# Performance work log

Hardware: AMD Instinct MI355X
Metric: run time of the kernel (lower is better)

## Reference

```python
import jax, jax.numpy as jnp
import numpy as np

K = 9
VOCAB = 7
DIM = 512
LOW = 256  # downsampled bottleneck dim
N_LAYERS = 2
EPS = 1e-5


def _inorm(x, g, b):
    # InstanceNorm1d over length axis (biased var), x: (N, C, K)
    m = jnp.mean(x, axis=-1, keepdims=True)
    v = jnp.mean((x - m) ** 2, axis=-1, keepdims=True)
    return g[None, :, None] * (x - m) * jax.lax.rsqrt(v + EPS) + b[None, :, None]


def _conv5_same(x, w, b):
    # x: (N, C, K), w: (O, C, 5), dilation 1, padding 'same' -> pad 2
    y = jax.lax.conv_general_dilated(
        x, w, window_strides=(1,), padding=[(2, 2)],
        dimension_numbers=('NCH', 'OIH', 'NCH'))
    return y + b[None, :, None]


def _bytenet_layer(x, p):
    (g1, b1, g2, b2, g3, b3, w1, c1b, w2, c2b, w3, c3b) = p
    h = jax.nn.gelu(_inorm(x, g1, b1), approximate=False)
    h = jnp.einsum('nck,oc->nok', h, w1) + c1b[None, :, None]      # 1x1 conv 512->256
    h = jax.nn.gelu(_inorm(h, g2, b2), approximate=False)
    h = _conv5_same(h, w2, c2b)                                     # k=5 conv 256->256
    h = jax.nn.gelu(_inorm(h, g3, b3), approximate=False)
    h = jnp.einsum('nck,oc->nok', h, w3) + c3b[None, :, None]      # 1x1 conv 256->512
    return h + x  # dropout is identity in eval


def setup_inputs() -> dict:
    key = jax.random.key(0)
    ks = jax.random.split(key, 16)
    x = jax.random.randint(ks[0], (8, 2048), 0, VOCAB)
    emb = jax.random.normal(ks[1], (VOCAB, DIM), jnp.float32) * 0.02
    emb = emb.at[6].set(0.0)  # padding_idx=6
    d = {
        'x': x,
        'emb': emb,
        'ln1_w': jnp.ones((N_LAYERS, DIM)), 'ln1_b': jnp.zeros((N_LAYERS, DIM)),
        'ln2_w': jnp.ones((N_LAYERS, LOW)), 'ln2_b': jnp.zeros((N_LAYERS, LOW)),
        'ln3_w': jnp.ones((N_LAYERS, LOW)), 'ln3_b': jnp.zeros((N_LAYERS, LOW)),
        'c1_w': jax.random.normal(ks[2], (N_LAYERS, LOW, DIM), jnp.float32) * 0.02,
        'c1_b': jnp.zeros((N_LAYERS, LOW)),
        'c2_w': jax.random.normal(ks[3], (N_LAYERS, LOW, LOW, 5), jnp.float32) * 0.02,
        'c2_b': jnp.zeros((N_LAYERS, LOW)),
        'c3_w': jax.random.normal(ks[4], (N_LAYERS, DIM, LOW), jnp.float32) * 0.02,
        'c3_b': jnp.zeros((N_LAYERS, DIM)),
        'out_w': jax.random.normal(ks[5], (VOCAB, DIM * K), jnp.float32) * 0.02,
        'out_b': jnp.zeros((VOCAB,)),
    }
    return d


def reference(x, emb, ln1_w, ln1_b, ln2_w, ln2_b, ln3_w, ln3_b,
              c1_w, c1_b, c2_w, c2_b, c3_w, c3_b, out_w, out_b):
    B, L = x.shape
    W = L - K + 1
    e = emb[x]                                        # (B, L, D)
    idx = jnp.arange(W)[:, None] + jnp.arange(K)      # (W, K)
    win = e[:, idx, :]                                # (B, W, K, D)
    h = win.transpose(0, 1, 3, 2).reshape(B * W, DIM, K)  # (N, D, K)
    for i in range(N_LAYERS):
        p = (ln1_w[i], ln1_b[i], ln2_w[i], ln2_b[i], ln3_w[i], ln3_b[i],
             c1_w[i], c1_b[i], c2_w[i], c2_b[i], c3_w[i], c3_b[i])
        h = _bytenet_layer(h, p)
    pred = h.reshape(B * W, DIM * K) @ out_w.T + out_b
    return pred.reshape(B, W, VOCAB)
```

## Files before the change

### kernel.cpp

```cpp
#include <hip/hip_runtime.h>

typedef __attribute__((ext_vector_type(8))) short bfv8;
typedef __attribute__((ext_vector_type(4))) float f32x4;
typedef __attribute__((ext_vector_type(4))) unsigned short usv4;

typedef __attribute__((address_space(1))) const void gvoid;
typedef __attribute__((address_space(3))) void lvoid;
__device__ __forceinline__ void gload16(const void* g, void* l) {
  __builtin_amdgcn_global_load_lds((gvoid*)g, (lvoid*)l, 16, 0, 0);
}

__device__ __forceinline__ float bf2f(unsigned short u) {
  union { unsigned int i; float f; } c; c.i = ((unsigned int)u) << 16; return c.f;
}
__device__ __forceinline__ unsigned short f2bf(float f) {
  union { float f; unsigned int i; } c; c.f = f;
  unsigned int r = c.i + 0x7FFFu + ((c.i >> 16) & 1u);
  return (unsigned short)(r >> 16);
}
__device__ __forceinline__ float gelu_(float x) {
  float z2 = 1.5957691216057308f * x * __builtin_fmaf(0.044715f, x * x, 1.0f);
  float e = __expf(z2);
  float t = __builtin_amdgcn_rcpf(e + 1.0f);
  return x - x * t;
}
__device__ __forceinline__ int div9(int col) {
  return (int)(__umulhi((unsigned)col, 954437177u) >> 1);
}

#define CHP 132
#define CHP2 66

__global__ void k_prep(const float* c1w, const float* c2w, const float* c3w,
                       const float* outw, unsigned short* W1b, unsigned short* W2t,
                       unsigned short* W3b, float* OWt) {
  int i = blockIdx.x * 256 + threadIdx.x;
  if (i < 262144) { W1b[i] = f2bf(c1w[i]); return; }
  i -= 262144;
  if (i < 655360) {
    int ii = i & 255, o = (i >> 8) & 255, rest = i >> 16;
    int t = rest % 5, l = rest / 5;
    W2t[i] = f2bf(c2w[(((l * 256 + o) << 8) + ii) * 5 + t]);
    return;
  }
  i -= 655360;
  if (i < 262144) { W3b[i] = f2bf(c3w[i]); return; }
  i -= 262144;
  if (i < 32256) {
    int c = i & 511, rk = i >> 9;
    int r = rk / 9, k = rk - 9 * r;
    OWt[i] = outw[r * 4608 + c * 9 + k];
  }
}

__global__ void k_pinit(const float* outb, float* pred) {
  int i = blockIdx.x * 256 + threadIdx.x;
  if (i < 114240) pred[i] = outb[i % 7];
}

__global__ void k_x0(const int* x, const float* emb, unsigned short* X, int n0) {
  int idx = blockIdx.x * 256 + threadIdx.x;
  int c4 = idx & 127, nl = idx >> 7;
  int gn = n0 + nl, b = gn >> 11, w = gn & 2047;
  unsigned short* dst = X + (size_t)(12 + nl * 12) * 512 + (c4 << 2);
  const int* xb = x + (b << 11);
  #pragma unroll
  for (int k = 0; k < 9; k++) {
    int t = w + k; if (t > 2047) t = 2047;
    const float* e = emb + xb[t] * 512 + (c4 << 2);
    float4 ev = *(const float4*)e;
    usv4 pk;
    pk[0] = f2bf(ev.x); pk[1] = f2bf(ev.y);
    pk[2] = f2bf(ev.z); pk[3] = f2bf(ev.w);
    *(usv4*)(dst + k * 512) = pk;
  }
}

__global__ void k_zpad(unsigned short* AL) {
  int i = threadIdx.x;
  for (; i < 12 * 256; i += 256) AL[i] = 0;
}

template <int MODE>
__global__ __launch_bounds__(512, 2) void k_gemm(
    const unsigned short* __restrict__ Aw, const unsigned short* __restrict__ Bsrc,
    const float* __restrict__ n1w, const float* __restrict__ n1b,
    const float* __restrict__ gw, const float* __restrict__ gb,
    unsigned short* __restrict__ Out, int nkc) {
  __shared__ __align__(16) unsigned short smem[69632];
  unsigned short* sE = smem;

  const int KROW = (MODE == 0) ? 512 : 256;
  const int KSTEPS = (MODE == 1) ? 20 : 8;
  int tid = threadIdx.x, wv = tid >> 6, ln = tid & 63;
  int lr = ln >> 3, lu = ln & 7;
  int swz = (lu ^ lr) << 3;
  int w0 = blockIdx.x << 5;
  int col0 = blockIdx.x * 288;

  int brow[5];
  #pragma unroll
  for (int s = 0; s < 5; s++) {
    int colg = col0 + (s << 6) + (wv << 3) + lr;
    if (colg >= nkc) colg = nkc - 1;
    brow[s] = colg + 3 * div9(colg) + 12;
  }

  f32x4 acc[4][9];
  #pragma unroll
  for (int i = 0; i < 4; i++)
    #pragma unroll
    for (int j = 0; j < 9; j++) acc[i][j] = (f32x4){0.f, 0.f, 0.f, 0.f};

  auto stage = [&](int buf, int ks) {
    int kb, dlt; const unsigned short* Ab;
    if (MODE == 1) {
      int t = ks % 5; kb = (ks / 5) << 6; dlt = t - 2; Ab = Aw + t * 65536;
    } else { kb = ks << 6; dlt = 0; Ab = Aw; }
    unsigned short* cA = smem + buf * 16384;
    unsigned short* cB = smem + 32768 + buf * 18432;
    #pragma unroll
    for (int p = 0; p < 4; p++) {
      int m = (p << 6) + (wv << 3) + lr;
      gload16(Ab + (size_t)m * KROW + kb + swz, cA + (p << 12) + (wv << 9));
    }
    #pragma unroll
    for (int s = 0; s < 4; s++)
      gload16(Bsrc + (size_t)(brow[s] + dlt) * KROW + kb + swz,
              cB + (s << 12) + (wv << 9));
    if (wv < 4)
      gload16(Bsrc + (size_t)(brow[4] + dlt) * KROW + kb + swz,
              cB + (4 << 12) + (wv << 9));
  };

  stage(0, 0);
  __syncthreads();

  int cur = 0;
  for (int ks = 0; ks < KSTEPS; ks++) {
    unsigned short* cA = smem + cur * 16384;
    unsigned short* cB = smem + 32768 + cur * 18432;

    if (MODE == 0) {
      int cg = tid & 15, win = tid >> 4;
      int u = cg >> 1, sub = (cg & 1) << 3;
      int gch = (ks << 6) + (cg << 2);
      float v[9][4], s1[4] = {0.f, 0.f, 0.f, 0.f};
      #pragma unroll
      for (int k = 0; k < 9; k++) {
        int cl = win * 9 + k;
        usv4 rv = *(const usv4*)((char*)cB + cl * 128 + ((u ^ (cl & 7)) << 4) + sub);
        #pragma unroll
        for (int j = 0; j < 4; j++) { v[k][j] = bf2f(rv[j]); s1[j] += v[k][j]; }
      }
      float mn[4], rr[4], gg[4], bo[4];
      #pragma unroll
      for (int j = 0; j < 4; j++) {
        mn[j] = s1[j] * (1.0f / 9.0f);
        float q = 0.f;
        #pragma unroll
        for (int k = 0; k < 9; k++) { float d = v[k][j] - mn[j]; q += d * d; }
        rr[j] = rsqrtf(q * (1.0f / 9.0f) + 1e-5f);
        gg[j] = n1w[gch + j]; bo[j] = n1b[gch + j];
      }
      #pragma unroll
      for (int k = 0; k < 9; k++) {
        int cl = win * 9 + k;
        usv4 pk;
        #pragma unroll
        for (int j = 0; j < 4; j++)
          pk[j] = f2bf(gelu_(gg[j] * (v[k][j] - mn[j]) * rr[j] + bo[j]));
        *(usv4*)((char*)cB + cl * 128 + ((u ^ (cl & 7)) << 4) + sub) = pk;
      }
      __syncthreads();
    }

    if (ks + 1 < KSTEPS) stage(cur ^ 1, ks + 1);

    int l16 = ln & 15, loct = ln >> 4;
    int wm = wv >> 1, wn = wv & 1;
    #pragma unroll
    for (int kk = 0; kk < 2; kk++) {
      int kbyte = (kk << 6) + (loct << 4);
      bfv8 af[4], bf_[9];
      #pragma unroll
      for (int mi = 0; mi < 4; mi++) {
        int row = (wm << 6) + (mi << 4) + l16;
        af[mi] = *(const bfv8*)((const char*)cA + row * 128 + (kbyte ^ ((row & 7) << 4)));
      }
      #pragma unroll
      for (int ni = 0; ni < 9; ni++) {
        int row = wn * 144 + (ni << 4) + l16;
        bf_[ni] = *(const bfv8*)((const char*)cB + row * 128 + (kbyte ^ ((row & 7) << 4)));
      }
      #pragma unroll
      for (int mi = 0; mi < 4; mi++)
        #pragma unroll
        for (int ni = 0; ni < 9; ni++)
          acc[mi][ni] = __builtin_amdgcn_mfma_f32_16x16x32_bf16(
              af[mi], bf_[ni], acc[mi][ni], 0, 0, 0);
    }
    __syncthreads();
    cur ^= 1;
  }

  int l16 = ln & 15, loct = ln >> 4;
  #pragma unroll
  for (int R = 0; R < 2; R++) {
    if (R) __syncthreads();
    if ((wv >> 2) == R) {
      int chh = (((wv >> 1) & 1) << 6) + (loct << 2);
      int colb = (wv & 1) * 144 + l16;
      #pragma unroll
      for (int mi = 0; mi < 4; mi++) {
        #pragma unroll
        for (int ni = 0; ni < 9; ni++) {
          usv4 pk;
          #pragma unroll
          for (int q = 0; q < 4; q++) pk[q] = f2bf(acc[mi][ni][q]);
          *(usv4*)(sE + (colb + (ni << 4)) * CHP + chh + (mi << 4)) = pk;
        }
      }
    }
    __syncthreads();
    #pragma unroll
    for (int tt = 0; tt < 2; tt++) {
      int t = tid + tt * 512;
      int c4 = t & 31, win = t >> 5;
      int chl = (R << 7) + (c4 << 2);
      const unsigned short* sb = sE + (win * 9) * CHP + (c4 << 2);
      size_t ob = (size_t)(12 + (size_t)(w0 + win) * 12) * 256 + chl;
      float s1[4] = {0.f, 0.f, 0.f, 0.f}, s2[4] = {0.f, 0.f, 0.f, 0.f};
      #pragma unroll
      for (int k = 0; k < 9; k++) {
        usv4 rv = *(const usv4*)(sb + k * CHP);
        #pragma unroll
        for (int j = 0; j < 4; j++) {
          float f = bf2f(rv[j]);
          s1[j] += f; s2[j] = __builtin_fmaf(f, f, s2[j]);
        }
      }
      float mn[4], rr[4], gg[4], bo[4];
      #pragma unroll
      for (int j = 0; j < 4; j++) {
        mn[j] = s1[j] * (1.0f / 9.0f);
        float var = s2[j] * (1.0f / 9.0f) - mn[j] * mn[j];
        rr[j] = rsqrtf(var + 1e-5f);
        gg[j] = gw[chl + j]; bo[j] = gb[chl + j];
      }
      #pragma unroll
      for (int k = 0; k < 9; k++) {
        usv4 rv = *(const usv4*)(sb + k * CHP);
        usv4 pk;
        #pragma unroll
        for (int j = 0; j < 4; j++)
          pk[j] = f2bf(gelu_(gg[j] * (bf2f(rv[j]) - mn[j]) * rr[j] + bo[j]));
        *(usv4*)(Out + ob + k * 256) = pk;
      }
      if (MODE == 0) {
        usv4 z = (usv4){0, 0, 0, 0};
        *(usv4*)(Out + ob + 9 * 256) = z;
        *(usv4*)(Out + ob + 10 * 256) = z;
        *(usv4*)(Out + ob + 11 * 256) = z;
      }
    }
  }
}

template <bool FOUT>
__global__ __launch_bounds__(256, 2) void k_gemm2(
    const unsigned short* __restrict__ Aw, const unsigned short* __restrict__ Bsrc,
    const float* __restrict__ cbias, unsigned short* __restrict__ Out, int nkc,
    const float* __restrict__ OWt, float* __restrict__ pred, int n0) {
  __shared__ __align__(16) unsigned short smem[34816];
  unsigned short* sE = smem;
  float* owl = (float*)((char*)smem + 19008);

  const int KROW = 256, KSTEPS = 4;
  int tid = threadIdx.x, wv = tid >> 6, ln = tid & 63;
  int lr = ln >> 3, lu = ln & 7;
  int swz = (lu ^ lr) << 3;
  int id = blockIdx.x;
  int slab = (id >> 3) & 3;
  int tile = ((id >> 5) << 3) | (id & 7);
  int m0 = slab << 7;
  int w0 = tile << 4;
  int col0 = tile * 144;

  int brow[5];
  #pragma unroll
  for (int s = 0; s < 5; s++) {
    int cl = (s < 4) ? ((s << 5) + (wv << 3) + lr) : (128 + (wv << 3) + lr);
    int colg = col0 + cl;
    if (colg >= nkc) colg = nkc - 1;
    brow[s] = colg + 3 * div9(colg) + 12;
  }
  const unsigned short* A0 = Aw + (size_t)m0 * KROW;

  f32x4 acc[2][9];
  #pragma unroll
  for (int i = 0; i < 2; i++)
    #pragma unroll
    for (int j = 0; j < 9; j++) acc[i][j] = (f32x4){0.f, 0.f, 0.f, 0.f};

  auto stage = [&](int buf, int ks) {
    int kb = ks << 6;
    unsigned short* cA = smem + buf * 8192;
    unsigned short* cB = smem + 16384 + buf * 9216;
    #pragma unroll
    for (int p = 0; p < 4; p++) {
      int m = (p << 5) + (wv << 3) + lr;
      gload16(A0 + (size_t)m * KROW + kb + swz, cA + ((p << 5) + (wv << 3)) * 64);
    }
    #pragma unroll
    for (int s = 0; s < 4; s++)
      gload16(Bsrc + (size_t)brow[s] * KROW + kb + swz,
              cB + ((s << 5) + (wv << 3)) * 64);
    if (wv < 2)
      gload16(Bsrc + (size_t)brow[4] * KROW + kb + swz,
              cB + (128 + (wv << 3)) * 64);
  };

  stage(0, 0);
  __syncthreads();

  int cur = 0;
  for (int ks = 0; ks < KSTEPS; ks++) {
    unsigned short* cA = smem + cur * 8192;
    unsigned short* cB = smem + 16384 + cur * 9216;
    if (ks + 1 < KSTEPS) stage(cur ^ 1, ks + 1);

    int l16 = ln & 15, loct = ln >> 4;
    #pragma unroll
    for (int kk = 0; kk < 2; kk++) {
      int kbyte = (kk << 6) + (loct << 4);
      bfv8 af[2], bf_[9];
      #pragma unroll
      for (int mi = 0; mi < 2; mi++) {
        int row = (wv << 5) + (mi << 4) + l16;
        af[mi] = *(const bfv8*)((const char*)cA + row * 128 + (kbyte ^ ((row & 7) << 4)));
      }
      #pragma unroll
      for (int ni = 0; ni < 9; ni++) {
        int row = (ni << 4) + l16;
        bf_[ni] = *(const bfv8*)((const char*)cB + row * 128 + (kbyte ^ ((row & 7) << 4)));
      }
      #pragma unroll
      for (int mi = 0; mi < 2; mi++)
        #pragma unroll
        for (int ni = 0; ni < 9; ni++)
          acc[mi][ni] = __builtin_amdgcn_mfma_f32_16x16x32_bf16(
              af[mi], bf_[ni], acc[mi][ni], 0, 0, 0);
    }
    __syncthreads();
    cur ^= 1;
  }

  if (FOUT) {
    #pragma unroll
    for (int i = 0; i < 8; i++) {
      int c = (i << 8) + tid;
      if (c < 2016)
        gload16(OWt + (size_t)(c >> 5) * 512 + m0 + ((c & 31) << 2),
                (char*)owl + c * 16);
    }
  }

  int l16 = ln & 15, loct = ln >> 4;
  int c4 = tid & 15, win = tid >> 4;
  #pragma unroll
  for (int R = 0; R < 2; R++) {
    if (R) __syncthreads();
    if ((wv >> 1) == R) {
      int chh = ((wv & 1) << 5) + (loct << 2);
      #pragma unroll
      for (int mi = 0; mi < 2; mi++) {
        #pragma unroll
        for (int ni = 0; ni < 9; ni++) {
          usv4 pk;
          #pragma unroll
          for (int q = 0; q < 4; q++) pk[q] = f2bf(acc[mi][ni][q]);
          *(usv4*)(sE + ((ni << 4) + l16) * CHP2 + chh + (mi << 4)) = pk;
        }
      }
    }
    __syncthreads();
    {
      int chg = m0 + (R << 6) + (c4 << 2);
      const unsigned short* sb = sE + (win * 9) * CHP2 + (c4 << 2);
      size_t ob = (size_t)(12 + (size_t)(w0 + win) * 12) * 512 + chg;
      float cb[4];
      #pragma unroll
      for (int j = 0; j < 4; j++) cb[j] = cbias[chg + j];
      if (!FOUT) {
        #pragma unroll
        for (int k = 0; k < 9; k++) {
          usv4 rv = *(const usv4*)(sb + k * CHP2);
          usv4 old = *(usv4*)(Out + ob + k * 512);
          usv4 pk;
          #pragma unroll
          for (int j = 0; j < 4; j++)
            pk[j] = f2bf(bf2f(rv[j]) + cb[j] + bf2f(old[j]));
          *(usv4*)(Out + ob + k * 512) = pk;
        }
      } else {
        float v[9][4];
        #pragma unroll
        for (int k = 0; k < 9; k++) {
          usv4 rv = *(const usv4*)(sb + k * CHP2);
          usv4 old = *(usv4*)(Out + ob + k * 512);
          #pragma unroll
          for (int j = 0; j < 4; j++)
            v[k][j] = bf2f(rv[j]) + cb[j] + bf2f(old[j]);
        }
        int gn = n0 + w0 + win, b = gn >> 11, w = gn & 2047;
        int cho = (R << 6) + (c4 << 2);
        #pragma unroll
        for (int r = 0; r < 7; r++) {
          float p = 0.f;
          #pragma unroll
          for (int k = 0; k < 9; k++) {
            float4 wvv = *(const float4*)(owl + (r * 9 + k) * 128 + cho);
            p = __builtin_fmaf(v[k][0], wvv.x, p);
            p = __builtin_fmaf(v[k][1], wvv.y, p);
            p = __builtin_fmaf(v[k][2], wvv.z, p);
            p = __builtin_fmaf(v[k][3], wvv.w, p);
          }
          p += __shfl_xor(p, 1);
          p += __shfl_xor(p, 2);
          p += __shfl_xor(p, 4);
          p += __shfl_xor(p, 8);
          if (c4 == 0 && w < 2040)
            atomicAdd(pred + (size_t)(b * 2040 + w) * 7 + r, p);
        }
      }
    }
  }
}

extern "C" void kernel_launch(void* const* d_in, const int* in_sizes, int n_in,
                              void* d_out, int out_size, void* d_ws, size_t ws_size,
                              hipStream_t stream) {
  const int*   x    = (const int*)d_in[0];
  const float* emb  = (const float*)d_in[1];
  const float* ln1w = (const float*)d_in[2];
  const float* ln1b = (const float*)d_in[3];
  const float* ln2w = (const float*)d_in[4];
  const float* ln2b = (const float*)d_in[5];
  const float* ln3w = (const float*)d_in[6];
  const float* ln3b = (const float*)d_in[7];
  const float* c1w  = (const float*)d_in[8];
  const float* c2w  = (const float*)d_in[10];
  const float* c3w  = (const float*)d_in[12];
  const float* c3b  = (const float*)d_in[13];
  const float* outw = (const float*)d_in[14];
  const float* outb = (const float*)d_in[15];
  float* pred = (float*)d_out;

  int nc = 8192;
  while (nc > 128 &&
         2488320ull + (unsigned long long)(nc + 1) * 24576ull > ws_size)
    nc >>= 1;
  int nkc = nc * 9;
  int tiles288 = nc >> 5;
  int tiles144 = nc >> 4;
  int nchunks = 16384 / nc;

  char* ws = (char*)d_ws;
  unsigned short* W1b = (unsigned short*)(ws);
  unsigned short* W2t = (unsigned short*)(ws + 524288);
  unsigned short* W3b = (unsigned short*)(ws + 1835008);
  float*          OWt = (float*)(ws + 2359296);
  char* act = ws + 2488320;
  size_t hiB = (size_t)(nc + 1) * 12288;
  size_t loB = (size_t)(nc + 1) * 6144;
  unsigned short* X   = (unsigned short*)(act);
  unsigned short* AL  = (unsigned short*)(act + hiB);
  unsigned short* AL2 = (unsigned short*)(act + hiB + loB);

  k_prep<<<(1211904 + 255) / 256, 256, 0, stream>>>(c1w, c2w, c3w, outw,
                                                    W1b, W2t, W3b, OWt);
  k_zpad<<<1, 256, 0, stream>>>(AL);
  k_pinit<<<(114240 + 255) / 256, 256, 0, stream>>>(outb, pred);

  for (int ch = 0; ch < nchunks; ch++) {
    int n0 = ch * nc;
    k_x0<<<nc / 2, 256, 0, stream>>>(x, emb, X, n0);
    for (int l = 0; l < 2; l++) {
      k_gemm<0><<<dim3(tiles288, 1), 512, 0, stream>>>(
          W1b + l * 131072, X, ln1w + l * 512, ln1b + l * 512,
          ln2w + l * 256, ln2b + l * 256, AL, nkc);
      k_gemm<1><<<dim3(tiles288, 1), 512, 0, stream>>>(
          W2t + l * 327680, AL, nullptr, nullptr,
          ln3w + l * 256, ln3b + l * 256, AL2, nkc);
      if (l == 0)
        k_gemm2<false><<<tiles144 * 4, 256, 0, stream>>>(
            W3b, AL2, c3b, X, nkc, nullptr, nullptr, 0);
      else
        k_gemm2<true><<<tiles144 * 4, 256, 0, stream>>>(
            W3b + 131072, AL2, c3b + 512, X, nkc, OWt, pred, n0);
    }
  }
}
```

Measured before the change: 717.5 us.

## Replace generic conv GEMM with dedicated k=5 conv kernel reusing staged activations

The k=5 convolution used to be a generic GEMM mode that restaged both weight and shifted activation tiles for each of the five taps, 20 K-steps in total. A new k_conv kernel stages one activation tile per 64-channel K chunk, with halo rows, into swizzled LDS. It then applies all five taps by shifting row indices and reads the weight fragments directly from global memory. The intent is to cut LDS staging traffic and sync count, in exchange for uncached-in-LDS weight reads from global/L2 and higher register use.

```diff
diff --git a/kernel.cpp b/kernel.cpp
--- a/kernel.cpp
+++ b/kernel.cpp
@@ -90,8 +90,8 @@
   __shared__ __align__(16) unsigned short smem[69632];
   unsigned short* sE = smem;
 
-  const int KROW = (MODE == 0) ? 512 : 256;
-  const int KSTEPS = (MODE == 1) ? 20 : 8;
+  const int KROW = 512;
+  const int KSTEPS = 8;
   int tid = threadIdx.x, wv = tid >> 6, ln = tid & 63;
   int lr = ln >> 3, lu = ln & 7;
   int swz = (lu ^ lr) << 3;
@@ -113,23 +113,20 @@
     for (int j = 0; j < 9; j++) acc[i][j] = (f32x4){0.f, 0.f, 0.f, 0.f};
 
   auto stage = [&](int buf, int ks) {
-    int kb, dlt; const unsigned short* Ab;
-    if (MODE == 1) {
-      int t = ks % 5; kb = (ks / 5) << 6; dlt = t - 2; Ab = Aw + t * 65536;
-    } else { kb = ks << 6; dlt = 0; Ab = Aw; }
+    int kb = ks << 6;
     unsigned short* cA = smem + buf * 16384;
     unsigned short* cB = smem + 32768 + buf * 18432;
     #pragma unroll
     for (int p = 0; p < 4; p++) {
       int m = (p << 6) + (wv << 3) + lr;
-      gload16(Ab + (size_t)m * KROW + kb + swz, cA + (p << 12) + (wv << 9));
+      gload16(Aw + (size_t)m * KROW + kb + swz, cA + (p << 12) + (wv << 9));
     }
     #pragma unroll
     for (int s = 0; s < 4; s++)
-      gload16(Bsrc + (size_t)(brow[s] + dlt) * KROW + kb + swz,
+      gload16(Bsrc + (size_t)brow[s] * KROW + kb + swz,
               cB + (s << 12) + (wv << 9));
     if (wv < 4)
-      gload16(Bsrc + (size_t)(brow[4] + dlt) * KROW + kb + swz,
+      gload16(Bsrc + (size_t)brow[4] * KROW + kb + swz,
               cB + (4 << 12) + (wv << 9));
   };
 
@@ -141,7 +138,7 @@
     unsigned short* cA = smem + cur * 16384;
     unsigned short* cB = smem + 32768 + cur * 18432;
 
-    if (MODE == 0) {
+    {
       int cg = tid & 15, win = tid >> 4;
       int u = cg >> 1, sub = (cg & 1) << 3;
       int gch = (ks << 6) + (cg << 2);
@@ -257,11 +254,152 @@
           pk[j] = f2bf(gelu_(gg[j] * (bf2f(rv[j]) - mn[j]) * rr[j] + bo[j]));
         *(usv4*)(Out + ob + k * 256) = pk;
       }
-      if (MODE == 0) {
+      {
         usv4 z = (usv4){0, 0, 0, 0};
         *(usv4*)(Out + ob + 9 * 256) = z;
         *(usv4*)(Out + ob + 10 * 256) = z;
         *(usv4*)(Out + ob + 11 * 256) = z;
+      }
+    }
+  }
+}
+
+__global__ __launch_bounds__(512, 2) void k_conv(
+    const unsigned short* __restrict__ W2, const unsigned short* __restrict__ ALs,
+    const float* __restrict__ gw, const float* __restrict__ gb,
+    unsigned short* __restrict__ Out) {
+  __shared__ __align__(16) unsigned short smem[49664];
+  unsigned short* sE = smem;
+
+  int tid = threadIdx.x, wv = tid >> 6, ln = tid & 63;
+  int l16 = ln & 15, loct = ln >> 4;
+  int wm = wv >> 1, wn = wv & 1;
+  int w0 = blockIdx.x << 5;
+  int grow0 = w0 * 12 + 10;
+
+  int r0[9];
+  #pragma unroll
+  for (int ni = 0; ni < 9; ni++) {
+    int lcol = wn * 144 + (ni << 4) + l16;
+    int wq = div9(lcol);
+    r0[ni] = wq * 12 + (lcol - wq * 9) + 2;
+  }
+
+  f32x4 acc[4][9];
+  #pragma unroll
+  for (int i = 0; i < 4; i++)
+    #pragma unroll
+    for (int j = 0; j < 9; j++) acc[i][j] = (f32x4){0.f, 0.f, 0.f, 0.f};
+
+  auto stage = [&](int buf, int kb) {
+    unsigned short* cB = smem + buf * 24832;
+    #pragma unroll
+    for (int p = 0; p < 6; p++) {
+      int c = tid + (p << 9);
+      int r = c >> 3, u = c & 7;
+      gload16(ALs + (size_t)(grow0 + r) * 256 + kb + ((u ^ (r & 7)) << 3),
+              cB + c * 8);
+    }
+    if (tid < 8) {
+      int c = 3072 + tid;
+      int r = c >> 3, u = c & 7;
+      gload16(ALs + (size_t)(grow0 + r) * 256 + kb + ((u ^ (r & 7)) << 3),
+              cB + c * 8);
+    }
+  };
+
+  stage(0, 0);
+  __syncthreads();
+
+  int cur = 0;
+  for (int kq = 0; kq < 4; kq++) {
+    unsigned short* cB = smem + cur * 24832;
+    int kb = kq << 6;
+    if (kq < 3) stage(cur ^ 1, (kq + 1) << 6);
+
+    #pragma unroll
+    for (int t = 0; t < 5; t++) {
+      const unsigned short* Wt = W2 + t * 65536;
+      int dlt = t - 2;
+      #pragma unroll
+      for (int kk = 0; kk < 2; kk++) {
+        bfv8 af[4], bf_[9];
+        #pragma unroll
+        for (int mi = 0; mi < 4; mi++) {
+          int row = (wm << 6) + (mi << 4) + l16;
+          af[mi] = *(const bfv8*)(Wt + (size_t)row * 256 + kb +
+                                  (kk << 5) + (loct << 3));
+        }
+        int kbyte = (kk << 6) + (loct << 4);
+        #pragma unroll
+        for (int ni = 0; ni < 9; ni++) {
+          int row = r0[ni] + dlt;
+          bf_[ni] = *(const bfv8*)((const char*)cB + row * 128 +
+                                   (kbyte ^ ((row & 7) << 4)));
+        }
+        #pragma unroll
+        for (int mi = 0; mi < 4; mi++)
+          #pragma unroll
+          for (int ni = 0; ni < 9; ni++)
+            acc[mi][ni] = __builtin_amdgcn_mfma_f32_16x16x32_bf16(
+                af[mi], bf_[ni], acc[mi][ni], 0, 0, 0);
+      }
+    }
+    __syncthreads();
+    cur ^= 1;
+  }
+
+  #pragma unroll
+  for (int R = 0; R < 2; R++) {
+    if (R) __syncthreads();
+    if ((wv >> 2) == R) {
+      int chh = (((wv >> 1) & 1) << 6) + (loct << 2);
+      int colb = (wv & 1) * 144 + l16;
+      #pragma unroll
+      for (int mi = 0; mi < 4; mi++) {
+        #pragma unroll
+        for (int ni = 0; ni < 9; ni++) {
+          usv4 pk;
+          #pragma unroll
+          for (int q = 0; q < 4; q++) pk[q] = f2bf(acc[mi][ni][q]);
+          *(usv4*)(sE + (colb + (ni << 4)) * CHP + chh + (mi << 4)) = pk;
+        }
+      }
+    }
+    __syncthreads();
+    #pragma unroll
+    for (int tt = 0; tt < 2; tt++) {
+      int t = tid + tt * 512;
+      int c4 = t & 31, win = t >> 5;
+      int chl = (R << 7) + (c4 << 2);
+      const unsigned short* sb = sE + (win * 9) * CHP + (c4 << 2);
+      size_t ob = (size_t)(12 + (size_t)(w0 + win) * 12) * 256 + chl;
+      float s1[4] = {0.f, 0.f, 0.f, 0.f}, s2[4] = {0.f, 0.f, 0.f, 0.f};
+      #pragma unroll
+      for (int k = 0; k < 9; k++) {
+        usv4 rv = *(const usv4*)(sb + k * CHP);
+        #pragma unroll
+        for (int j = 0; j < 4; j++) {
+          float f = bf2f(rv[j]);
+          s1[j] += f; s2[j] = __builtin_fmaf(f, f, s2[j]);
+        }
+      }
+      float mn[4], rr[4], gg[4], bo[4];
+      #pragma unroll
+      for (int j = 0; j < 4; j++) {
+        mn[j] = s1[j] * (1.0f / 9.0f);
+        float var = s2[j] * (1.0f / 9.0f) - mn[j] * mn[j];
+        rr[j] = rsqrtf(var + 1e-5f);
+        gg[j] = gw[chl + j]; bo[j] = gb[chl + j];
+      }
+      #pragma unroll
+      for (int k = 0; k < 9; k++) {
+        usv4 rv = *(const usv4*)(sb + k * CHP);
+        usv4 pk;
+        #pragma unroll
+        for (int j = 0; j < 4; j++)
+          pk[j] = f2bf(gelu_(gg[j] * (bf2f(rv[j]) - mn[j]) * rr[j] + bo[j]));
+        *(usv4*)(Out + ob + k * 256) = pk;
       }
     }
   }
@@ -490,9 +628,8 @@
       k_gemm<0><<<dim3(tiles288, 1), 512, 0, stream>>>(
           W1b + l * 131072, X, ln1w + l * 512, ln1b + l * 512,
           ln2w + l * 256, ln2b + l * 256, AL, nkc);
-      k_gemm<1><<<dim3(tiles288, 1), 512, 0, stream>>>(
-          W2t + l * 327680, AL, nullptr, nullptr,
-          ln3w + l * 256, ln3b + l * 256, AL2, nkc);
+      k_conv<<<tiles288, 512, 0, stream>>>(
+          W2t + l * 327680, AL, ln3w + l * 256, ln3b + l * 256, AL2);
       if (l == 0)
         k_gemm2<false><<<tiles144 * 4, 256, 0, stream>>>(
             W3b, AL2, c3b, X, nkc, nullptr, nullptr, 0);
```

Result: slower. 1.331 ms (+85.5%).
